# Kernel tuning notes

Hardware: AMD Instinct MI355X
Metric: run time of the kernel (lower is better)

The kernel has to match this reference:

```python
import jax, jax.numpy as jnp
import numpy as np

B, L, H, G = 16, 1024, 1024, 128


def setup_inputs() -> dict:
    key = jax.random.key(0)
    ks = jax.random.split(key, 6)
    s = 0.02
    return {
        "events": jax.random.normal(ks[0], (B, L, H), jnp.float32),
        "contexts": jax.random.normal(ks[1], (B, L - 1, H), jnp.float32),
        "Wzm": jax.random.normal(ks[2], (2 * H, G), jnp.float32) * s,
        "bzm": jnp.zeros((G,), jnp.float32),
        "Wzv": jax.random.normal(ks[3], (2 * H, G), jnp.float32) * s,
        "bzv": jnp.zeros((G,), jnp.float32),
        "Wqm": jax.random.normal(ks[4], (3 * H, G), jnp.float32) * s,
        "bqm": jnp.zeros((G,), jnp.float32),
        "Wqv": jax.random.normal(ks[5], (3 * H, G), jnp.float32) * s,
        "bqv": jnp.zeros((G,), jnp.float32),
    }


def reference(events, contexts, Wzm, bzm, Wzv, bzv, Wqm, bqm, Wqv, bqv):
    # adjacent event pairs: [B, L-1, 2H]
    ep = jnp.concatenate([events[:, :-1, :], events[:, 1:, :]], axis=-1)
    z_mean = ep @ Wzm + bzm          # [B, L-1, G]
    z_log_var = ep @ Wzv + bzv
    ce = jnp.concatenate([ep, contexts], axis=-1)  # [B, L-1, 3H]
    q_z_mean = ce @ Wqm + bqm
    q_z_log_var = ce @ Wqv + bqv
    # closed-form KL(p || q) for diagonal Gaussians, summed over G per (b, pair)
    kl = 0.5 * jnp.sum(
        q_z_log_var - z_log_var
        + (jnp.exp(z_log_var) + (z_mean - q_z_mean) ** 2) * jnp.exp(-q_z_log_var)
        - 1.0,
        axis=-1,
    )  # [B, L-1]
    kl_loss = jnp.mean(kl).reshape(1)  # sum over (b, pair) / (B * (L-1))
    return (z_mean, z_log_var, q_z_mean, q_z_log_var, kl_loss)
```

## Files before the change

kernel.cpp:

```cpp
#include <hip/hip_runtime.h>
#include <stdint.h>

typedef unsigned short u16;
typedef __attribute__((ext_vector_type(8))) short short8;
typedef __attribute__((ext_vector_type(4))) float f32x4;
typedef __attribute__((ext_vector_type(2))) uint32_t u32x2;
typedef __attribute__((ext_vector_type(2))) float f32x2;

#define B_      16
#define L_      1024
#define H_      1024
#define G_      128
#define M_TOT   16368
#define K_TOT   3072
#define OUT_SEG 2095104
#define KL_IDX  (4*OUT_SEG)
#define KL_BLOCKS 4092

#define WS_WT_OFF    0
#define WS_BIAS_OFF  3145728
#define WS_PART_OFF  3147776

__device__ inline u16 f2bf(float f) {
    union { float f; uint32_t u; } x; x.f = f;
    uint32_t u = x.u;
    return (u16)((u + 0x7fffu + ((u >> 16) & 1u)) >> 16);
}

__device__ inline void gload16(const void* g, void* l) {
    __builtin_amdgcn_global_load_lds(
        (const __attribute__((address_space(1))) void*)g,
        (__attribute__((address_space(3))) void*)l, 16, 0, 0);
}

__global__ __launch_bounds__(256) void prep_kernel(
    const float* __restrict__ Wzm, const float* __restrict__ bzm,
    const float* __restrict__ Wzv, const float* __restrict__ bzv,
    const float* __restrict__ Wqm, const float* __restrict__ bqm,
    const float* __restrict__ Wqv, const float* __restrict__ bqv,
    u16* __restrict__ wt, float* __restrict__ bias)
{
    const int ng = blockIdx.x >> 2;
    const int kq = blockIdx.x & 3;
    const int n0 = ng * 8;
    const float* W; const float* bsrc; int g0; int kmax;
    if (n0 < 128)      { W = Wzm; bsrc = bzm; g0 = n0;       kmax = 2048; }
    else if (n0 < 256) { W = Wzv; bsrc = bzv; g0 = n0 - 128; kmax = 2048; }
    else if (n0 < 384) { W = Wqm; bsrc = bqm; g0 = n0 - 256; kmax = 3072; }
    else               { W = Wqv; bsrc = bqv; g0 = n0 - 384; kmax = 3072; }
    const int tid = threadIdx.x;
    if (kq == 0 && tid < 8) bias[n0 + tid] = bsrc[g0 + tid];

    __shared__ float lt[8][260];
    const int go = tid & 7;
    const int kk = tid >> 3;
    const int nn = tid >> 5;
    const int kc = (tid & 31) * 8;

    for (int i = 0; i < 3; ++i) {
        int kbase = kq * 768 + i * 256;
        __syncthreads();
        #pragma unroll
        for (int kk2 = 0; kk2 < 8; ++kk2) {
            int k = kbase + kk2 * 32 + kk;
            float v = (k < kmax) ? W[(size_t)k * G_ + g0 + go] : 0.0f;
            lt[go][kk2 * 32 + kk] = v;
        }
        __syncthreads();
        union { short8 s; u16 u[8]; } o;
        #pragma unroll
        for (int j = 0; j < 8; ++j) o.u[j] = f2bf(lt[nn][kc + j]);
        *(short8*)&wt[(size_t)(n0 + nn) * K_TOT + kbase + kc] = o.s;
    }
}

__global__ __launch_bounds__(256, 2) void gemm_kernel(
    const float* __restrict__ events, const float* __restrict__ contexts,
    const u16* __restrict__ wt, const float* __restrict__ bias,
    float* __restrict__ out)
{
    __shared__ u16 Ab[2][128 * 64];
    __shared__ u16 Bs[2][128 * 64];

    const int tid = threadIdx.x;
    const int bid = blockIdx.x;
    const int xx  = bid & 7;
    const int jj  = bid >> 3;
    const int nb  = jj & 3;
    const int mp  = (jj >> 2) * 8 + xx;
    const int m0  = mp * 128;

    const int lane = tid & 63;
    const int w    = tid >> 6;
    const int wm   = (w >> 1) * 64;
    const int wn   = (w & 1) * 64;
    const int lr   = lane & 15;
    const int kg   = lane >> 4;

    const int r0 = tid >> 2;
    const int q  = tid & 3;
    const float* paE[2]; const float* paC[2];
    int aw[2][4];
    #pragma unroll
    for (int g = 0; g < 2; ++g) {
        int r = r0 + g * 64;
        int m = m0 + r; if (m > M_TOT - 1) m = M_TOT - 1;
        int b = m / 1023;
        int t = m - b * 1023;
        paE[g] = events   + ((size_t)(b * L_ + t)) * H_;
        paC[g] = contexts + ((size_t)(b * (L_ - 1) + t)) * H_;
        #pragma unroll
        for (int j = 0; j < 4; ++j)
            aw[g][j] = r * 64 + (((2 * j + (q >> 1)) ^ (r & 7)) << 3)
                     + (q & 1) * 4;
    }

    const u16* bS[4];
    #pragma unroll
    for (int it = 0; it < 4; ++it) {
        int c  = it * 256 + tid;
        int v  = c >> 3;
        int cs = (c & 7) ^ (v & 7);
        bS[it] = wt + (size_t)(nb * 128 + v) * K_TOT + cs * 8;
    }

    int aoff[4][2], boff[4][2];
    #pragma unroll
    for (int i = 0; i < 4; ++i) {
        int row = wm + i * 16 + lr;
        int nn  = wn + i * 16 + lr;
        #pragma unroll
        for (int ks = 0; ks < 2; ++ks) {
            aoff[i][ks] = row * 64 + (((ks * 4 + kg) ^ (row & 7)) << 3);
            boff[i][ks] = nn  * 64 + (((ks * 4 + kg) ^ (nn  & 7)) << 3);
        }
    }

    f32x4 acc[4][4];
    #pragma unroll
    for (int i = 0; i < 4; ++i)
        #pragma unroll
        for (int j = 0; j < 4; ++j)
            acc[i][j] = (f32x4){0.f, 0.f, 0.f, 0.f};

    auto stageB = [&](int buf, int kt) {
        int k0 = kt * 64;
        #pragma unroll
        for (int it = 0; it < 4; ++it)
            gload16(bS[it] + k0, &Bs[buf][(it * 256 + tid) * 8]);
    };
    auto compute = [&](int buf) {
        #pragma unroll
        for (int ks = 0; ks < 2; ++ks) {
            short8 a[4], bf[4];
            #pragma unroll
            for (int i = 0; i < 4; ++i)
                a[i] = *(const short8*)&Ab[buf][aoff[i][ks]];
            #pragma unroll
            for (int j = 0; j < 4; ++j)
                bf[j] = *(const short8*)&Bs[buf][boff[j][ks]];
            __builtin_amdgcn_s_setprio(1);
            #pragma unroll
            for (int i = 0; i < 4; ++i)
                #pragma unroll
                for (int j = 0; j < 4; ++j)
                    acc[i][j] = __builtin_amdgcn_mfma_f32_16x16x32_bf16(
                        a[i], bf[j], acc[i][j], 0, 0, 0);
            __builtin_amdgcn_s_setprio(0);
        }
    };

    f32x4 P0, P1, P2, P3, P4, P5, P6, P7;
    f32x4 Q0, Q1, Q2, Q3, Q4, Q5, Q6, Q7;

#define LOADA(p, KT)                                                           \
    {                                                                          \
        int k0_ = (KT) * 64;                                                   \
        int rg_ = (KT) >> 4;                                                   \
        int kq_ = (k0_ & 1023) + q * 4;                                        \
        const float* s0_ = (rg_ == 0) ? paE[0]                                 \
                          : (rg_ == 1 ? (paE[0] + H_) : paC[0]);               \
        const float* s1_ = (rg_ == 0) ? paE[1]                                 \
                          : (rg_ == 1 ? (paE[1] + H_) : paC[1]);               \
        s0_ += kq_; s1_ += kq_;                                                \
        p##0 = *(const f32x4*)(s0_ +  0);                                      \
        p##1 = *(const f32x4*)(s0_ + 16);                                      \
        p##2 = *(const f32x4*)(s0_ + 32);                                      \
        p##3 = *(const f32x4*)(s0_ + 48);                                      \
        p##4 = *(const f32x4*)(s1_ +  0);                                      \
        p##5 = *(const f32x4*)(s1_ + 16);                                      \
        p##6 = *(const f32x4*)(s1_ + 32);                                      \
        p##7 = *(const f32x4*)(s1_ + 48);                                      \
    }
#define CVT1(p, RI, G, J, BUF)                                                 \
    {                                                                          \
        uint32_t lo_, hi_;                                                     \
        asm("v_cvt_pk_bf16_f32 %0, %1, %2" : "=v"(lo_) : "v"(p##RI[0]), "v"(p##RI[1])); \
        asm("v_cvt_pk_bf16_f32 %0, %1, %2" : "=v"(hi_) : "v"(p##RI[2]), "v"(p##RI[3])); \
        *(u32x2*)&Ab[BUF][aw[G][J]] = (u32x2){lo_, hi_};                       \
    }
#define CVTW(p, BUF)                                                           \
    CVT1(p, 0, 0, 0, BUF) CVT1(p, 1, 0, 1, BUF)                                \
    CVT1(p, 2, 0, 2, BUF) CVT1(p, 3, 0, 3, BUF)                                \
    CVT1(p, 4, 1, 0, BUF) CVT1(p, 5, 1, 1, BUF)                                \
    CVT1(p, 6, 1, 2, BUF) CVT1(p, 7, 1, 3, BUF)

#define WAITV(N)                                                               \
    asm volatile("s_waitcnt vmcnt(" #N ")" ::: "memory");                      \
    __builtin_amdgcn_sched_barrier(0);
#define LGKM0                                                                  \
    asm volatile("s_waitcnt lgkmcnt(0)" ::: "memory");                         \
    __builtin_amdgcn_sched_barrier(0);
#define BAR __builtin_amdgcn_s_barrier()

    LOADA(P, 0);
    stageB(0, 0);
    WAITV(4);
    CVTW(P, 0);
    LOADA(Q, 1);
    LGKM0;

    for (int t = 0; t < 46; t += 2) {
        LOADA(P, t + 2);
        stageB(1, t + 1);
        WAITV(12); BAR;
        compute(0);
        CVTW(Q, 1);
        LGKM0; BAR;
        LOADA(Q, t + 3);
        stageB(0, t + 2);
        WAITV(12); BAR;
        compute(1);
        CVTW(P, 0);
        LGKM0; BAR;
    }
    stageB(1, 47);
    WAITV(4); BAR;
    compute(0);
    CVTW(Q, 1);
    LGKM0; BAR;
    WAITV(0); BAR;
    compute(1);

#undef LOADA
#undef CVT1
#undef CVTW
#undef WAITV
#undef LGKM0
#undef BAR

    const float* bptr = bias + nb * 128;
    float* obase = out + (size_t)nb * OUT_SEG;
    #pragma unroll
    for (int i = 0; i < 4; ++i) {
        int mloc = wm + i * 16 + kg * 4;
        #pragma unroll
        for (int j = 0; j < 4; ++j) {
            int g = wn + j * 16 + lr;
            float bv = bptr[g];
            #pragma unroll
            for (int rr = 0; rr < 4; ++rr) {
                int mo = m0 + mloc + rr;
                if (mo < M_TOT) obase[(size_t)mo * G_ + g] = acc[i][j][rr] + bv;
            }
        }
    }
}

__global__ __launch_bounds__(256) void kl_kernel(const float* __restrict__ out,
                                                 float* __restrict__ partial)
{
    int wid  = threadIdx.x >> 6;
    int row  = blockIdx.x * 4 + wid;
    int lane = threadIdx.x & 63;
    const float* zm  = out;
    const float* zlv = out + OUT_SEG;
    const float* qm  = out + (size_t)2 * OUT_SEG;
    const float* qlv = out + (size_t)3 * OUT_SEG;
    size_t base = (size_t)row * G_ + lane * 2;
    f32x2 a = *(const f32x2*)&zm[base];
    f32x2 b = *(const f32x2*)&zlv[base];
    f32x2 c = *(const f32x2*)&qm[base];
    f32x2 d = *(const f32x2*)&qlv[base];
    float s = 0.f;
    #pragma unroll
    for (int e = 0; e < 2; ++e) {
        float diff = a[e] - c[e];
        s += d[e] - b[e] + (__expf(b[e]) + diff * diff) * __expf(-d[e]) - 1.0f;
    }
    #pragma unroll
    for (int off = 32; off > 0; off >>= 1)
        s += __shfl_down(s, off);
    __shared__ float pw[4];
    if (lane == 0) pw[wid] = s;
    __syncthreads();
    if (threadIdx.x == 0)
        partial[blockIdx.x] = pw[0] + pw[1] + pw[2] + pw[3];
}

__global__ __launch_bounds__(256) void kl_final(const float* __restrict__ partial,
                                                float* __restrict__ out)
{
    float s = 0.f;
    for (int i = threadIdx.x; i < KL_BLOCKS; i += 256) s += partial[i];
    #pragma unroll
    for (int off = 32; off > 0; off >>= 1)
        s += __shfl_down(s, off);
    __shared__ float pw[4];
    int wid = threadIdx.x >> 6;
    int lane = threadIdx.x & 63;
    if (lane == 0) pw[wid] = s;
    __syncthreads();
    if (threadIdx.x == 0)
        out[KL_IDX] = 0.5f * (pw[0] + pw[1] + pw[2] + pw[3]) / (float)M_TOT;
}

extern "C" void kernel_launch(void* const* d_in, const int* in_sizes, int n_in,
                              void* d_out, int out_size, void* d_ws, size_t ws_size,
                              hipStream_t stream)
{
    const float* events   = (const float*)d_in[0];
    const float* contexts = (const float*)d_in[1];
    const float* Wzm = (const float*)d_in[2];
    const float* bzm = (const float*)d_in[3];
    const float* Wzv = (const float*)d_in[4];
    const float* bzv = (const float*)d_in[5];
    const float* Wqm = (const float*)d_in[6];
    const float* bqm = (const float*)d_in[7];
    const float* Wqv = (const float*)d_in[8];
    const float* bqv = (const float*)d_in[9];
    float* out = (float*)d_out;

    u16*   wt      = (u16*)((char*)d_ws + WS_WT_OFF);
    float* bias    = (float*)((char*)d_ws + WS_BIAS_OFF);
    float* partial = (float*)((char*)d_ws + WS_PART_OFF);

    prep_kernel<<<256, 256, 0, stream>>>(Wzm, bzm, Wzv, bzv, Wqm, bqm, Wqv, bqv,
                                         wt, bias);
    gemm_kernel<<<512, 256, 0, stream>>>(events, contexts, wt, bias, out);
    kl_kernel<<<KL_BLOCKS, 256, 0, stream>>>(out, partial);
    kl_final<<<1, 256, 0, stream>>>(partial, out);
}
```

Measured before the change: 95.79 us.

## Use four-stage K=32 LDS pipeline in GEMM and widen KL loads

The GEMM main loop moves from a double-buffered K=64 tile to a four-buffer ring of K=32 tiles with a new swizzled LDS layout that packs two rows per 64-element line. Loads for tile t+2 are issued while tile t is computed, with one barrier per phase instead of two. Fewer A registers are held per stage, and the aim is better overlap of global loads with MFMA work. The KL kernel now uses float4 loads over 8 rows per block, which halves the block count.

```diff
diff --git a/kernel.cpp b/kernel.cpp
--- a/kernel.cpp
+++ b/kernel.cpp
@@ -4,8 +4,6 @@
 typedef unsigned short u16;
 typedef __attribute__((ext_vector_type(8))) short short8;
 typedef __attribute__((ext_vector_type(4))) float f32x4;
-typedef __attribute__((ext_vector_type(2))) uint32_t u32x2;
-typedef __attribute__((ext_vector_type(2))) float f32x2;
 
 #define B_      16
 #define L_      1024
@@ -15,7 +13,7 @@
 #define K_TOT   3072
 #define OUT_SEG 2095104
 #define KL_IDX  (4*OUT_SEG)
-#define KL_BLOCKS 4092
+#define KL_BLOCKS 2046
 
 #define WS_WT_OFF    0
 #define WS_BIAS_OFF  3145728
@@ -79,8 +77,8 @@
     const u16* __restrict__ wt, const float* __restrict__ bias,
     float* __restrict__ out)
 {
-    __shared__ u16 Ab[2][128 * 64];
-    __shared__ u16 Bs[2][128 * 64];
+    __shared__ u16 Ab[4][64 * 64];
+    __shared__ u16 Bs[4][64 * 64];
 
     const int tid = threadIdx.x;
     const int bid = blockIdx.x;
@@ -97,43 +95,36 @@
     const int lr   = lane & 15;
     const int kg   = lane >> 4;
 
-    const int r0 = tid >> 2;
-    const int q  = tid & 3;
-    const float* paE[2]; const float* paC[2];
-    int aw[2][4];
-    #pragma unroll
-    for (int g = 0; g < 2; ++g) {
-        int r = r0 + g * 64;
-        int m = m0 + r; if (m > M_TOT - 1) m = M_TOT - 1;
-        int b = m / 1023;
-        int t = m - b * 1023;
-        paE[g] = events   + ((size_t)(b * L_ + t)) * H_;
-        paC[g] = contexts + ((size_t)(b * (L_ - 1) + t)) * H_;
-        #pragma unroll
-        for (int j = 0; j < 4; ++j)
-            aw[g][j] = r * 64 + (((2 * j + (q >> 1)) ^ (r & 7)) << 3)
-                     + (q & 1) * 4;
-    }
-
-    const u16* bS[4];
-    #pragma unroll
-    for (int it = 0; it < 4; ++it) {
-        int c  = it * 256 + tid;
-        int v  = c >> 3;
-        int cs = (c & 7) ^ (v & 7);
-        bS[it] = wt + (size_t)(nb * 128 + v) * K_TOT + cs * 8;
-    }
-
-    int aoff[4][2], boff[4][2];
+    const int r = tid >> 1;
+    const int h = tid & 1;
+    int m = m0 + r; if (m > M_TOT - 1) m = M_TOT - 1;
+    int bb = m / 1023;
+    int tt = m - bb * 1023;
+    const float* paE = events   + ((size_t)(bb * L_ + tt)) * H_;
+    const float* paC = contexts + ((size_t)(bb * (L_ - 1) + tt)) * H_;
+    const int srA  = r >> 1;
+    const int aw0  = srA * 64 + ((((r & 1) * 4 + 2 * h)     ^ (srA & 7)) << 3);
+    const int aw1  = srA * 64 + ((((r & 1) * 4 + 2 * h + 1) ^ (srA & 7)) << 3);
+
+    const u16* bS[2];
+    #pragma unroll
+    for (int it = 0; it < 2; ++it) {
+        int cl = it * 256 + tid;
+        int sr = cl >> 3;
+        int cp = cl & 7;
+        int c  = cp ^ (sr & 7);
+        int v  = sr * 2 + (c >> 2);
+        int kc = c & 3;
+        bS[it] = wt + (size_t)(nb * 128 + v) * K_TOT + kc * 8;
+    }
+
+    int aoff[4], boff[4];
     #pragma unroll
     for (int i = 0; i < 4; ++i) {
         int row = wm + i * 16 + lr;
+        aoff[i] = (row >> 1) * 64 + ((((row & 1) * 4 + kg) ^ ((row >> 1) & 7)) << 3);
         int nn  = wn + i * 16 + lr;
-        #pragma unroll
-        for (int ks = 0; ks < 2; ++ks) {
-            aoff[i][ks] = row * 64 + (((ks * 4 + kg) ^ (row & 7)) << 3);
-            boff[i][ks] = nn  * 64 + (((ks * 4 + kg) ^ (nn  & 7)) << 3);
-        }
+        boff[i] = (nn >> 1) * 64 + ((((nn & 1) * 4 + kg) ^ ((nn >> 1) & 7)) << 3);
     }
 
     f32x4 acc[4][4];
@@ -143,67 +134,55 @@
         for (int j = 0; j < 4; ++j)
             acc[i][j] = (f32x4){0.f, 0.f, 0.f, 0.f};
 
-    auto stageB = [&](int buf, int kt) {
-        int k0 = kt * 64;
-        #pragma unroll
-        for (int it = 0; it < 4; ++it)
-            gload16(bS[it] + k0, &Bs[buf][(it * 256 + tid) * 8]);
-    };
-    auto compute = [&](int buf) {
-        #pragma unroll
-        for (int ks = 0; ks < 2; ++ks) {
-            short8 a[4], bf[4];
-            #pragma unroll
-            for (int i = 0; i < 4; ++i)
-                a[i] = *(const short8*)&Ab[buf][aoff[i][ks]];
-            #pragma unroll
-            for (int j = 0; j < 4; ++j)
-                bf[j] = *(const short8*)&Bs[buf][boff[j][ks]];
-            __builtin_amdgcn_s_setprio(1);
-            #pragma unroll
-            for (int i = 0; i < 4; ++i)
-                #pragma unroll
-                for (int j = 0; j < 4; ++j)
-                    acc[i][j] = __builtin_amdgcn_mfma_f32_16x16x32_bf16(
-                        a[i], bf[j], acc[i][j], 0, 0, 0);
-            __builtin_amdgcn_s_setprio(0);
-        }
-    };
-
-    f32x4 P0, P1, P2, P3, P4, P5, P6, P7;
-    f32x4 Q0, Q1, Q2, Q3, Q4, Q5, Q6, Q7;
+    f32x4 P0, P1, P2, P3;
+    f32x4 Q0, Q1, Q2, Q3;
 
 #define LOADA(p, KT)                                                           \
     {                                                                          \
-        int k0_ = (KT) * 64;                                                   \
-        int rg_ = (KT) >> 4;                                                   \
-        int kq_ = (k0_ & 1023) + q * 4;                                        \
-        const float* s0_ = (rg_ == 0) ? paE[0]                                 \
-                          : (rg_ == 1 ? (paE[0] + H_) : paC[0]);               \
-        const float* s1_ = (rg_ == 0) ? paE[1]                                 \
-                          : (rg_ == 1 ? (paE[1] + H_) : paC[1]);               \
-        s0_ += kq_; s1_ += kq_;                                                \
-        p##0 = *(const f32x4*)(s0_ +  0);                                      \
-        p##1 = *(const f32x4*)(s0_ + 16);                                      \
-        p##2 = *(const f32x4*)(s0_ + 32);                                      \
-        p##3 = *(const f32x4*)(s0_ + 48);                                      \
-        p##4 = *(const f32x4*)(s1_ +  0);                                      \
-        p##5 = *(const f32x4*)(s1_ + 16);                                      \
-        p##6 = *(const f32x4*)(s1_ + 32);                                      \
-        p##7 = *(const f32x4*)(s1_ + 48);                                      \
-    }
-#define CVT1(p, RI, G, J, BUF)                                                 \
+        int rg_ = (KT) >> 5;                                                   \
+        int kq_ = (((KT) & 31) << 5) + h * 16;                                 \
+        const float* s_ = (rg_ == 0) ? paE : (rg_ == 1 ? (paE + H_) : paC);    \
+        s_ += kq_;                                                             \
+        p##0 = *(const f32x4*)(s_ +  0);                                       \
+        p##1 = *(const f32x4*)(s_ +  4);                                       \
+        p##2 = *(const f32x4*)(s_ +  8);                                       \
+        p##3 = *(const f32x4*)(s_ + 12);                                       \
+    }
+#define STAGEB(BUF, KT)                                                        \
     {                                                                          \
-        uint32_t lo_, hi_;                                                     \
-        asm("v_cvt_pk_bf16_f32 %0, %1, %2" : "=v"(lo_) : "v"(p##RI[0]), "v"(p##RI[1])); \
-        asm("v_cvt_pk_bf16_f32 %0, %1, %2" : "=v"(hi_) : "v"(p##RI[2]), "v"(p##RI[3])); \
-        *(u32x2*)&Ab[BUF][aw[G][J]] = (u32x2){lo_, hi_};                       \
+        gload16(bS[0] + (KT) * 32, &Bs[BUF][tid * 8]);                         \
+        gload16(bS[1] + (KT) * 32, &Bs[BUF][(256 + tid) * 8]);                 \
     }
 #define CVTW(p, BUF)                                                           \
-    CVT1(p, 0, 0, 0, BUF) CVT1(p, 1, 0, 1, BUF)                                \
-    CVT1(p, 2, 0, 2, BUF) CVT1(p, 3, 0, 3, BUF)                                \
-    CVT1(p, 4, 1, 0, BUF) CVT1(p, 5, 1, 1, BUF)                                \
-    CVT1(p, 6, 1, 2, BUF) CVT1(p, 7, 1, 3, BUF)
+    {                                                                          \
+        union { short8 v; uint32_t u[4]; } w0_, w1_;                           \
+        asm("v_cvt_pk_bf16_f32 %0, %1, %2" : "=v"(w0_.u[0]) : "v"(p##0[0]), "v"(p##0[1])); \
+        asm("v_cvt_pk_bf16_f32 %0, %1, %2" : "=v"(w0_.u[1]) : "v"(p##0[2]), "v"(p##0[3])); \
+        asm("v_cvt_pk_bf16_f32 %0, %1, %2" : "=v"(w0_.u[2]) : "v"(p##1[0]), "v"(p##1[1])); \
+        asm("v_cvt_pk_bf16_f32 %0, %1, %2" : "=v"(w0_.u[3]) : "v"(p##1[2]), "v"(p##1[3])); \
+        asm("v_cvt_pk_bf16_f32 %0, %1, %2" : "=v"(w1_.u[0]) : "v"(p##2[0]), "v"(p##2[1])); \
+        asm("v_cvt_pk_bf16_f32 %0, %1, %2" : "=v"(w1_.u[1]) : "v"(p##2[2]), "v"(p##2[3])); \
+        asm("v_cvt_pk_bf16_f32 %0, %1, %2" : "=v"(w1_.u[2]) : "v"(p##3[0]), "v"(p##3[1])); \
+        asm("v_cvt_pk_bf16_f32 %0, %1, %2" : "=v"(w1_.u[3]) : "v"(p##3[2]), "v"(p##3[3])); \
+        *(short8*)&Ab[BUF][aw0] = w0_.v;                                       \
+        *(short8*)&Ab[BUF][aw1] = w1_.v;                                       \
+    }
+#define COMPUTE(BUF)                                                           \
+    {                                                                          \
+        short8 a_[4], b_[4];                                                   \
+        _Pragma("unroll")                                                      \
+        for (int i = 0; i < 4; ++i) a_[i] = *(const short8*)&Ab[BUF][aoff[i]]; \
+        _Pragma("unroll")                                                      \
+        for (int j = 0; j < 4; ++j) b_[j] = *(const short8*)&Bs[BUF][boff[j]]; \
+        __builtin_amdgcn_s_setprio(1);                                         \
+        _Pragma("unroll")                                                      \
+        for (int i = 0; i < 4; ++i)                                            \
+            _Pragma("unroll")                                                  \
+            for (int j = 0; j < 4; ++j)                                        \
+                acc[i][j] = __builtin_amdgcn_mfma_f32_16x16x32_bf16(           \
+                    a_[i], b_[j], acc[i][j], 0, 0, 0);                         \
+        __builtin_amdgcn_s_setprio(0);                                         \
+    }
 
 #define WAITV(N)                                                               \
     asm volatile("s_waitcnt vmcnt(" #N ")" ::: "memory");                      \
@@ -211,43 +190,47 @@
 #define LGKM0                                                                  \
     asm volatile("s_waitcnt lgkmcnt(0)" ::: "memory");                         \
     __builtin_amdgcn_sched_barrier(0);
-#define BAR __builtin_amdgcn_s_barrier()
+#define BARS                                                                   \
+    __builtin_amdgcn_s_barrier();                                              \
+    __builtin_amdgcn_sched_barrier(0);
+
+#define PHASE(KT, BC, BV, BS2, PL, PC)                                         \
+    LOADA(PL, (KT) + 2);                                                       \
+    STAGEB(BS2, (KT) + 2);                                                     \
+    WAITV(8); LGKM0; BARS;                                                     \
+    COMPUTE(BC);                                                               \
+    CVTW(PC, BV);
 
     LOADA(P, 0);
-    stageB(0, 0);
-    WAITV(4);
+    STAGEB(0, 0);
+    WAITV(2);
     CVTW(P, 0);
     LOADA(Q, 1);
+    STAGEB(1, 1);
     LGKM0;
 
-    for (int t = 0; t < 46; t += 2) {
-        LOADA(P, t + 2);
-        stageB(1, t + 1);
-        WAITV(12); BAR;
-        compute(0);
-        CVTW(Q, 1);
-        LGKM0; BAR;
-        LOADA(Q, t + 3);
-        stageB(0, t + 2);
-        WAITV(12); BAR;
-        compute(1);
-        CVTW(P, 0);
-        LGKM0; BAR;
-    }
-    stageB(1, 47);
-    WAITV(4); BAR;
-    compute(0);
-    CVTW(Q, 1);
-    LGKM0; BAR;
-    WAITV(0); BAR;
-    compute(1);
-
+    for (int t = 0; t < 92; t += 4) {
+        PHASE(t,     0, 1, 2, P, Q);
+        PHASE(t + 1, 1, 2, 3, Q, P);
+        PHASE(t + 2, 2, 3, 0, P, Q);
+        PHASE(t + 3, 3, 0, 1, Q, P);
+    }
+    PHASE(92, 0, 1, 2, P, Q);
+    PHASE(93, 1, 2, 3, Q, P);
+    WAITV(2); LGKM0; BARS;
+    COMPUTE(2);
+    CVTW(Q, 3);
+    WAITV(0); LGKM0; BARS;
+    COMPUTE(3);
+
+#undef PHASE
 #undef LOADA
-#undef CVT1
+#undef STAGEB
 #undef CVTW
+#undef COMPUTE
 #undef WAITV
 #undef LGKM0
-#undef BAR
+#undef BARS
 
     const float* bptr = bias + nb * 128;
     float* obase = out + (size_t)nb * OUT_SEG;
@@ -270,21 +253,20 @@
 __global__ __launch_bounds__(256) void kl_kernel(const float* __restrict__ out,
                                                  float* __restrict__ partial)
 {
-    int wid  = threadIdx.x >> 6;
-    int row  = blockIdx.x * 4 + wid;
-    int lane = threadIdx.x & 63;
+    int row  = blockIdx.x * 8 + (threadIdx.x >> 5);
+    int col  = (threadIdx.x & 31) * 4;
     const float* zm  = out;
     const float* zlv = out + OUT_SEG;
     const float* qm  = out + (size_t)2 * OUT_SEG;
     const float* qlv = out + (size_t)3 * OUT_SEG;
-    size_t base = (size_t)row * G_ + lane * 2;
-    f32x2 a = *(const f32x2*)&zm[base];
-    f32x2 b = *(const f32x2*)&zlv[base];
-    f32x2 c = *(const f32x2*)&qm[base];
-    f32x2 d = *(const f32x2*)&qlv[base];
+    size_t base = (size_t)row * G_ + col;
+    f32x4 a = *(const f32x4*)&zm[base];
+    f32x4 b = *(const f32x4*)&zlv[base];
+    f32x4 c = *(const f32x4*)&qm[base];
+    f32x4 d = *(const f32x4*)&qlv[base];
     float s = 0.f;
     #pragma unroll
-    for (int e = 0; e < 2; ++e) {
+    for (int e = 0; e < 4; ++e) {
         float diff = a[e] - c[e];
         s += d[e] - b[e] + (__expf(b[e]) + diff * diff) * __expf(-d[e]) - 1.0f;
     }
@@ -292,6 +274,8 @@
     for (int off = 32; off > 0; off >>= 1)
         s += __shfl_down(s, off);
     __shared__ float pw[4];
+    int wid  = threadIdx.x >> 6;
+    int lane = threadIdx.x & 63;
     if (lane == 0) pw[wid] = s;
     __syncthreads();
     if (threadIdx.x == 0)
```

New measurement: 106.9 us. 1.12x slower.

## Use 512-thread GEMM blocks with 8 waves and widen KL kernel loads

Applied to the files above, without the earlier changes.

The GEMM block grows from 4 to 8 waves. Each wave now computes a 64x32 sub-tile, and each thread stages one A row and two B chunks per k-step, which halves per-thread register and load pressure and gives more latency hiding per CU. The vmcnt waits are rescaled to match the smaller number of in-flight loads. Separately, the KL kernel processes 8 rows per block with float4 loads, so it launches half as many blocks. The cost is fewer MFMAs per LDS fragment read, since B fragments are reused across only 2 columns instead of 4, and the 2-blocks-per-CU bound with 512 threads may limit registers.

```diff
diff --git a/kernel.cpp b/kernel.cpp
--- a/kernel.cpp
+++ b/kernel.cpp
@@ -5,7 +5,6 @@
 typedef __attribute__((ext_vector_type(8))) short short8;
 typedef __attribute__((ext_vector_type(4))) float f32x4;
 typedef __attribute__((ext_vector_type(2))) uint32_t u32x2;
-typedef __attribute__((ext_vector_type(2))) float f32x2;
 
 #define B_      16
 #define L_      1024
@@ -15,7 +14,7 @@
 #define K_TOT   3072
 #define OUT_SEG 2095104
 #define KL_IDX  (4*OUT_SEG)
-#define KL_BLOCKS 4092
+#define KL_BLOCKS 2046
 
 #define WS_WT_OFF    0
 #define WS_BIAS_OFF  3145728
@@ -74,7 +73,7 @@
     }
 }
 
-__global__ __launch_bounds__(256, 2) void gemm_kernel(
+__global__ __launch_bounds__(512, 2) void gemm_kernel(
     const float* __restrict__ events, const float* __restrict__ contexts,
     const u16* __restrict__ wt, const float* __restrict__ bias,
     float* __restrict__ out)
@@ -92,118 +91,104 @@
 
     const int lane = tid & 63;
     const int w    = tid >> 6;
-    const int wm   = (w >> 1) * 64;
-    const int wn   = (w & 1) * 64;
+    const int wm   = (w >> 2) * 64;
+    const int wn   = (w & 3) * 32;
     const int lr   = lane & 15;
     const int kg   = lane >> 4;
 
-    const int r0 = tid >> 2;
-    const int q  = tid & 3;
-    const float* paE[2]; const float* paC[2];
-    int aw[2][4];
-    #pragma unroll
-    for (int g = 0; g < 2; ++g) {
-        int r = r0 + g * 64;
-        int m = m0 + r; if (m > M_TOT - 1) m = M_TOT - 1;
-        int b = m / 1023;
-        int t = m - b * 1023;
-        paE[g] = events   + ((size_t)(b * L_ + t)) * H_;
-        paC[g] = contexts + ((size_t)(b * (L_ - 1) + t)) * H_;
-        #pragma unroll
-        for (int j = 0; j < 4; ++j)
-            aw[g][j] = r * 64 + (((2 * j + (q >> 1)) ^ (r & 7)) << 3)
-                     + (q & 1) * 4;
-    }
-
-    const u16* bS[4];
-    #pragma unroll
-    for (int it = 0; it < 4; ++it) {
-        int c  = it * 256 + tid;
+    const int r = tid >> 2;
+    const int q = tid & 3;
+    int m = m0 + r; if (m > M_TOT - 1) m = M_TOT - 1;
+    int bb = m / 1023;
+    int tt = m - bb * 1023;
+    const float* paE = events   + ((size_t)(bb * L_ + tt)) * H_;
+    const float* paC = contexts + ((size_t)(bb * (L_ - 1) + tt)) * H_;
+    int aw[4];
+    #pragma unroll
+    for (int j = 0; j < 4; ++j)
+        aw[j] = r * 64 + (((2 * j + (q >> 1)) ^ (r & 7)) << 3) + (q & 1) * 4;
+
+    const u16* bS[2];
+    #pragma unroll
+    for (int it = 0; it < 2; ++it) {
+        int c  = it * 512 + tid;
         int v  = c >> 3;
         int cs = (c & 7) ^ (v & 7);
         bS[it] = wt + (size_t)(nb * 128 + v) * K_TOT + cs * 8;
     }
 
-    int aoff[4][2], boff[4][2];
+    int aoff[4][2], boff[2][2];
     #pragma unroll
     for (int i = 0; i < 4; ++i) {
         int row = wm + i * 16 + lr;
-        int nn  = wn + i * 16 + lr;
-        #pragma unroll
-        for (int ks = 0; ks < 2; ++ks) {
+        #pragma unroll
+        for (int ks = 0; ks < 2; ++ks)
             aoff[i][ks] = row * 64 + (((ks * 4 + kg) ^ (row & 7)) << 3);
-            boff[i][ks] = nn  * 64 + (((ks * 4 + kg) ^ (nn  & 7)) << 3);
-        }
-    }
-
-    f32x4 acc[4][4];
+    }
+    #pragma unroll
+    for (int j = 0; j < 2; ++j) {
+        int nn = wn + j * 16 + lr;
+        #pragma unroll
+        for (int ks = 0; ks < 2; ++ks)
+            boff[j][ks] = nn * 64 + (((ks * 4 + kg) ^ (nn & 7)) << 3);
+    }
+
+    f32x4 acc[4][2];
     #pragma unroll
     for (int i = 0; i < 4; ++i)
         #pragma unroll
-        for (int j = 0; j < 4; ++j)
+        for (int j = 0; j < 2; ++j)
             acc[i][j] = (f32x4){0.f, 0.f, 0.f, 0.f};
 
     auto stageB = [&](int buf, int kt) {
         int k0 = kt * 64;
-        #pragma unroll
-        for (int it = 0; it < 4; ++it)
-            gload16(bS[it] + k0, &Bs[buf][(it * 256 + tid) * 8]);
+        gload16(bS[0] + k0, &Bs[buf][tid * 8]);
+        gload16(bS[1] + k0, &Bs[buf][(512 + tid) * 8]);
     };
     auto compute = [&](int buf) {
         #pragma unroll
         for (int ks = 0; ks < 2; ++ks) {
-            short8 a[4], bf[4];
+            short8 a[4], bf[2];
             #pragma unroll
             for (int i = 0; i < 4; ++i)
                 a[i] = *(const short8*)&Ab[buf][aoff[i][ks]];
             #pragma unroll
-            for (int j = 0; j < 4; ++j)
+            for (int j = 0; j < 2; ++j)
                 bf[j] = *(const short8*)&Bs[buf][boff[j][ks]];
             __builtin_amdgcn_s_setprio(1);
             #pragma unroll
             for (int i = 0; i < 4; ++i)
                 #pragma unroll
-                for (int j = 0; j < 4; ++j)
+                for (int j = 0; j < 2; ++j)
                     acc[i][j] = __builtin_amdgcn_mfma_f32_16x16x32_bf16(
                         a[i], bf[j], acc[i][j], 0, 0, 0);
             __builtin_amdgcn_s_setprio(0);
         }
     };
 
-    f32x4 P0, P1, P2, P3, P4, P5, P6, P7;
-    f32x4 Q0, Q1, Q2, Q3, Q4, Q5, Q6, Q7;
+    f32x4 P0, P1, P2, P3;
+    f32x4 Q0, Q1, Q2, Q3;
 
 #define LOADA(p, KT)                                                           \
     {                                                                          \
         int k0_ = (KT) * 64;                                                   \
         int rg_ = (KT) >> 4;                                                   \
         int kq_ = (k0_ & 1023) + q * 4;                                        \
-        const float* s0_ = (rg_ == 0) ? paE[0]                                 \
-                          : (rg_ == 1 ? (paE[0] + H_) : paC[0]);               \
-        const float* s1_ = (rg_ == 0) ? paE[1]                                 \
-                          : (rg_ == 1 ? (paE[1] + H_) : paC[1]);               \
-        s0_ += kq_; s1_ += kq_;                                                \
-        p##0 = *(const f32x4*)(s0_ +  0);                                      \
-        p##1 = *(const f32x4*)(s0_ + 16);                                      \
-        p##2 = *(const f32x4*)(s0_ + 32);                                      \
-        p##3 = *(const f32x4*)(s0_ + 48);                                      \
-        p##4 = *(const f32x4*)(s1_ +  0);                                      \
-        p##5 = *(const f32x4*)(s1_ + 16);                                      \
-        p##6 = *(const f32x4*)(s1_ + 32);                                      \
-        p##7 = *(const f32x4*)(s1_ + 48);                                      \
-    }
-#define CVT1(p, RI, G, J, BUF)                                                 \
+        const float* s_ = (rg_ == 0) ? paE : (rg_ == 1 ? (paE + H_) : paC);    \
+        s_ += kq_;                                                             \
+        p##0 = *(const f32x4*)(s_ +  0);                                       \
+        p##1 = *(const f32x4*)(s_ + 16);                                       \
+        p##2 = *(const f32x4*)(s_ + 32);                                       \
+        p##3 = *(const f32x4*)(s_ + 48);                                       \
+    }
+#define CVT1(p, J, BUF)                                                        \
     {                                                                          \
         uint32_t lo_, hi_;                                                     \
-        asm("v_cvt_pk_bf16_f32 %0, %1, %2" : "=v"(lo_) : "v"(p##RI[0]), "v"(p##RI[1])); \
-        asm("v_cvt_pk_bf16_f32 %0, %1, %2" : "=v"(hi_) : "v"(p##RI[2]), "v"(p##RI[3])); \
-        *(u32x2*)&Ab[BUF][aw[G][J]] = (u32x2){lo_, hi_};                       \
-    }
-#define CVTW(p, BUF)                                                           \
-    CVT1(p, 0, 0, 0, BUF) CVT1(p, 1, 0, 1, BUF)                                \
-    CVT1(p, 2, 0, 2, BUF) CVT1(p, 3, 0, 3, BUF)                                \
-    CVT1(p, 4, 1, 0, BUF) CVT1(p, 5, 1, 1, BUF)                                \
-    CVT1(p, 6, 1, 2, BUF) CVT1(p, 7, 1, 3, BUF)
+        asm("v_cvt_pk_bf16_f32 %0, %1, %2" : "=v"(lo_) : "v"(p##J[0]), "v"(p##J[1])); \
+        asm("v_cvt_pk_bf16_f32 %0, %1, %2" : "=v"(hi_) : "v"(p##J[2]), "v"(p##J[3])); \
+        *(u32x2*)&Ab[BUF][aw[J]] = (u32x2){lo_, hi_};                          \
+    }
+#define CVTW(p, BUF)  CVT1(p, 0, BUF) CVT1(p, 1, BUF) CVT1(p, 2, BUF) CVT1(p, 3, BUF)
 
 #define WAITV(N)                                                               \
     asm volatile("s_waitcnt vmcnt(" #N ")" ::: "memory");                      \
@@ -215,7 +200,7 @@
 
     LOADA(P, 0);
     stageB(0, 0);
-    WAITV(4);
+    WAITV(2);
     CVTW(P, 0);
     LOADA(Q, 1);
     LGKM0;
@@ -223,19 +208,19 @@
     for (int t = 0; t < 46; t += 2) {
         LOADA(P, t + 2);
         stageB(1, t + 1);
-        WAITV(12); BAR;
+        WAITV(6); BAR;
         compute(0);
         CVTW(Q, 1);
         LGKM0; BAR;
         LOADA(Q, t + 3);
         stageB(0, t + 2);
-        WAITV(12); BAR;
+        WAITV(6); BAR;
         compute(1);
         CVTW(P, 0);
         LGKM0; BAR;
     }
     stageB(1, 47);
-    WAITV(4); BAR;
+    WAITV(2); BAR;
     compute(0);
     CVTW(Q, 1);
     LGKM0; BAR;
@@ -255,7 +240,7 @@
     for (int i = 0; i < 4; ++i) {
         int mloc = wm + i * 16 + kg * 4;
         #pragma unroll
-        for (int j = 0; j < 4; ++j) {
+        for (int j = 0; j < 2; ++j) {
             int g = wn + j * 16 + lr;
             float bv = bptr[g];
             #pragma unroll
@@ -270,21 +255,20 @@
 __global__ __launch_bounds__(256) void kl_kernel(const float* __restrict__ out,
                                                  float* __restrict__ partial)
 {
-    int wid  = threadIdx.x >> 6;
-    int row  = blockIdx.x * 4 + wid;
-    int lane = threadIdx.x & 63;
+    int row  = blockIdx.x * 8 + (threadIdx.x >> 5);
+    int col  = (threadIdx.x & 31) * 4;
     const float* zm  = out;
     const float* zlv = out + OUT_SEG;
     const float* qm  = out + (size_t)2 * OUT_SEG;
     const float* qlv = out + (size_t)3 * OUT_SEG;
-    size_t base = (size_t)row * G_ + lane * 2;
-    f32x2 a = *(const f32x2*)&zm[base];
-    f32x2 b = *(const f32x2*)&zlv[base];
-    f32x2 c = *(const f32x2*)&qm[base];
-    f32x2 d = *(const f32x2*)&qlv[base];
+    size_t base = (size_t)row * G_ + col;
+    f32x4 a = *(const f32x4*)&zm[base];
+    f32x4 b = *(const f32x4*)&zlv[base];
+    f32x4 c = *(const f32x4*)&qm[base];
+    f32x4 d = *(const f32x4*)&qlv[base];
     float s = 0.f;
     #pragma unroll
-    for (int e = 0; e < 2; ++e) {
+    for (int e = 0; e < 4; ++e) {
         float diff = a[e] - c[e];
         s += d[e] - b[e] + (__expf(b[e]) + diff * diff) * __expf(-d[e]) - 1.0f;
     }
@@ -292,6 +276,8 @@
     for (int off = 32; off > 0; off >>= 1)
         s += __shfl_down(s, off);
     __shared__ float pw[4];
+    int wid  = threadIdx.x >> 6;
+    int lane = threadIdx.x & 63;
     if (lane == 0) pw[wid] = s;
     __syncthreads();
     if (threadIdx.x == 0)
@@ -337,7 +323,7 @@
 
     prep_kernel<<<256, 256, 0, stream>>>(Wzm, bzm, Wzv, bzv, Wqm, bqm, Wqv, bqv,
                                          wt, bias);
-    gemm_kernel<<<512, 256, 0, stream>>>(events, contexts, wt, bias, out);
+    gemm_kernel<<<512, 512, 0, stream>>>(events, contexts, wt, bias, out);
     kl_kernel<<<KL_BLOCKS, 256, 0, stream>>>(out, partial);
     kl_final<<<1, 256, 0, stream>>>(partial, out);
 }
```

New measurement: 94.47 us, median of 2. No clear change (-1.4%).
